# Kernel optimization log

Measured on AMD Instinct MI355X. Metric: run time of the kernel, lower is better.

The kernel has to match this reference:

```python
import jax, jax.numpy as jnp
import numpy as np

D_MODEL = 256
KSIZE = 16
EPS = 1e-5


def conv1d(x, w, b):
    # x: [B, C, N], w: [O, C, K], SAME padding over node axis
    y = jax.lax.conv_general_dilated(x, w, window_strides=(1,), padding='SAME',
                                     dimension_numbers=('NCH', 'OIH', 'NCH'))
    return y + b[None, :, None]


def layernorm(x, g, b):
    mu = jnp.mean(x, axis=-1, keepdims=True)
    var = jnp.mean(jnp.square(x - mu), axis=-1, keepdims=True)
    return (x - mu) * jax.lax.rsqrt(var + EPS) * g + b


def setup_inputs() -> dict:
    key = jax.random.key(0)
    ks = jax.random.split(key, 16)
    B, N, d, K = 4, 2048, D_MODEL, KSIZE
    conv_scale = 1.0 / np.sqrt(d * K)
    lin_scale = 1.0 / np.sqrt(d)
    return {
        'src': jax.random.normal(ks[0], (B, N, d), jnp.float32),
        'x_lst': jnp.zeros((B, N, N), jnp.float32),
        'adj': jax.random.randint(ks[1], (B, N, N), 0, 2, jnp.int32),
        'dis': jax.random.uniform(ks[2], (B, N, N), jnp.float32),
        'Wq': jax.random.normal(ks[3], (d, d, K), jnp.float32) * conv_scale,
        'bq': jnp.zeros((d,), jnp.float32),
        'Wk': jax.random.normal(ks[4], (d, d, K), jnp.float32) * conv_scale,
        'bk': jnp.zeros((d,), jnp.float32),
        'Wv': jax.random.normal(ks[5], (d, d, K), jnp.float32) * conv_scale,
        'bv': jnp.zeros((d,), jnp.float32),
        'W1': jax.random.normal(ks[6], (d, d), jnp.float32) * lin_scale,
        'b1': jnp.zeros((d,), jnp.float32),
        'W2': jax.random.normal(ks[7], (d, d), jnp.float32) * lin_scale,
        'b2': jnp.zeros((d,), jnp.float32),
        'W3': jax.random.normal(ks[8], (d, d), jnp.float32) * lin_scale,
        'b3': jnp.zeros((d,), jnp.float32),
        'g1': jnp.ones((d,), jnp.float32),
        'be1': jnp.zeros((d,), jnp.float32),
        'g2': jnp.ones((d,), jnp.float32),
        'be2': jnp.zeros((d,), jnp.float32),
    }


def reference(src, x_lst, adj, dis, Wq, bq, Wk, bk, Wv, bv,
              W1, b1, W2, b2, W3, b3, g1, be1, g2, be2):
    # ---- _ga_block: transpose to channel-major, graph attention ----
    x = jnp.swapaxes(src, -2, -1)                      # [B, d, N]
    q = conv1d(x, Wq, bq)                              # [B, d, N]
    k = conv1d(x, Wk, bk)
    v = conv1d(x, Wv, bv)
    scale = 1.0 / jnp.sqrt(jnp.asarray(D_MODEL, src.dtype))
    scores = jnp.einsum('bdn,bdm->bnm', q, k) * scale  # [B, N, N]
    scores = scores - dis                              # distance bias
    scores = jnp.where(adj > 0, scores, jnp.asarray(-1e9, scores.dtype))
    attn = jax.nn.softmax(scores, axis=-1)             # [B, N, N]
    x_lst_new = x_lst + attn                           # accumulated attention state
    out = jnp.einsum('bnm,bdm->bdn', attn, v)          # [B, d, N]
    x1 = jnp.swapaxes(out, -2, -1)                     # [B, N, d] (dropout = identity in eval)
    # ---- residual + norm1 ----
    h = layernorm(src + x1, g1, be1)
    # ---- 3-layer LeakyReLU MLP + residual + norm2 ----
    m = jax.nn.leaky_relu(h @ W1.T + b1)
    m = jax.nn.leaky_relu(m @ W2.T + b2)
    m = m @ W3.T + b3
    h = layernorm(h + m, g2, be2)
    return h, x_lst_new
```

## Files before the change

kernel.cpp:

```cpp
#include <hip/hip_runtime.h>
#include <stdint.h>

typedef _Float16 h16;
typedef _Float16 h8v __attribute__((ext_vector_type(8)));
typedef float    f4v __attribute__((ext_vector_type(4)));
typedef int      i4v __attribute__((ext_vector_type(4)));

#define NBATCH 4
#define NNODE  2048
#define DM     256
#define NPAD   2063
#define PARTN  (8192 * 256)

__device__ __forceinline__ void async16(const void* g, void* l) {
#if __has_builtin(__builtin_amdgcn_global_load_lds)
  __builtin_amdgcn_global_load_lds((__attribute__((address_space(1))) void*)g,
                                   (__attribute__((address_space(3))) void*)l, 16, 0, 0);
#else
  *(f4v*)l = *(const f4v*)g;
#endif
}

__device__ __forceinline__ void gemm_tile(
    const h16* Abase, int astride,
    const h16* Bbase, int bstride,
    h16* As, h16* Bs, f4v acc[4][4], int kiters)
{
  const int tid  = threadIdx.x;
  const int lane = tid & 63;
  const int wv   = tid >> 6;
  const int srow = tid >> 2;
  const int sch  = ((tid & 3) ^ ((tid >> 3) & 3)) * 8;
  const h16* gA0 = Abase + (long)srow * astride + sch;
  const h16* gA1 = Abase + (long)(srow + 64) * astride + sch;
  const h16* gB0 = Bbase + (long)srow * bstride + sch;
  const h16* gB1 = Bbase + (long)(srow + 64) * bstride + sch;
  h16* lA0 = As + tid * 8;
  h16* lA1 = As + 2048 + tid * 8;
  h16* lB0 = Bs + tid * 8;
  h16* lB1 = Bs + 2048 + tid * 8;
  const int swz = ((lane & 15) >> 1) & 3;
  const int qq  = ((lane >> 4) ^ swz) * 8;
  const int amr = ((wv & 1) * 64 + (lane & 15)) * 32 + qq;
  const int bnr = ((wv >> 1) * 64 + (lane & 15)) * 32 + qq;

  async16(gA0, lA0); async16(gA1, lA1);
  async16(gB0, lB0); async16(gB1, lB1);

  for (int kt = 0; kt < kiters; ++kt) {
    asm volatile("s_waitcnt vmcnt(0)" ::: "memory");
    __syncthreads();
    const int cur = (kt & 1) << 12;
    if (kt + 1 < kiters) {
      const int nxt = (~kt & 1) << 12;
      const int k0 = (kt + 1) * 32;
      async16(gA0 + k0, lA0 + nxt); async16(gA1 + k0, lA1 + nxt);
      async16(gB0 + k0, lB0 + nxt); async16(gB1 + k0, lB1 + nxt);
    }
    h8v af[4], bf[4];
#pragma unroll
    for (int i = 0; i < 4; ++i) af[i] = *(const h8v*)(As + cur + amr + i * 512);
#pragma unroll
    for (int j = 0; j < 4; ++j) bf[j] = *(const h8v*)(Bs + cur + bnr + j * 512);
#pragma unroll
    for (int i = 0; i < 4; ++i)
#pragma unroll
      for (int j = 0; j < 4; ++j)
        acc[i][j] = __builtin_amdgcn_mfma_f32_16x16x32_f16(af[i], bf[j], acc[i][j], 0, 0, 0);
  }
}

__device__ __forceinline__ void zero_acc(f4v acc[4][4]) {
#pragma unroll
  for (int i = 0; i < 4; ++i)
#pragma unroll
    for (int j = 0; j < 4; ++j) {
      f4v z = {0.f, 0.f, 0.f, 0.f};
      acc[i][j] = z;
    }
}

__global__ void prep_src_kernel(const float* __restrict__ src, h16* __restrict__ Xpad) {
  int idx = blockIdx.x * 256 + threadIdx.x;
  int c = idx & 255;
  int row = idx >> 8;
  int b = row / NPAD;
  int n = row - b * NPAD;
  float v = 0.f;
  int ns = n - 7;
  if (ns >= 0 && ns < NNODE) v = src[((long)b * NNODE + ns) * DM + c];
  Xpad[idx] = (h16)v;
}

__global__ void prep_wconv_kernel(const float* __restrict__ Wq, const float* __restrict__ Wk,
                                  const float* __restrict__ Wv, h16* __restrict__ Wt) {
  int idx = blockIdx.x * 256 + threadIdx.x;
  int w = idx >> 20;
  int rem = idx & 1048575;
  int o = rem >> 12;
  int tc = rem & 4095;
  int t = tc >> 8;
  int c = tc & 255;
  const float* W = (w == 0) ? Wq : (w == 1) ? Wk : Wv;
  Wt[idx] = (h16)W[(o * 256 + c) * 16 + t];
}

__global__ void prep_wlin_kernel(const float* __restrict__ W1, const float* __restrict__ W2,
                                 const float* __restrict__ W3, h16* __restrict__ Wl) {
  int idx = blockIdx.x * 256 + threadIdx.x;
  int w = idx >> 16;
  int rem = idx & 65535;
  const float* W = (w == 0) ? W1 : (w == 1) ? W2 : W3;
  Wl[idx] = (h16)W[rem];
}

__global__ __launch_bounds__(256) void conv_gemm_kernel(
    const h16* __restrict__ Xpad, const h16* __restrict__ Wt,
    const float* __restrict__ bq, const float* __restrict__ bk, const float* __restrict__ bv,
    h16* __restrict__ Q, h16* __restrict__ Ko, h16* __restrict__ Vt)
{
  __shared__ __align__(16) h16 As[8192];
  __shared__ __align__(16) h16 Bs[8192];
  const int mt = blockIdx.x, ct = blockIdx.y, w = blockIdx.z;
  const int m0 = mt * 128;
  const int b = m0 >> 11, n0 = m0 & 2047;
  const h16* Abase = Xpad + ((long)(b * NPAD + n0)) * DM;
  const h16* Bbase = Wt + (long)w * (256 * 4096) + (long)ct * 128 * 4096;
  f4v acc[4][4];
  zero_acc(acc);
  gemm_tile(Abase, DM, Bbase, 4096, As, Bs, acc, 128);

  const float* bias = (w == 0) ? bq : (w == 1) ? bk : bv;
  const int lane = threadIdx.x & 63, wv = threadIdx.x >> 6;
  const int rbase = (wv & 1) * 64 + (lane >> 4) * 4;
  const int cbase = (wv >> 1) * 64 + (lane & 15);
#pragma unroll
  for (int j = 0; j < 4; ++j) {
    const int gc = ct * 128 + cbase + j * 16;
    const float bias_v = bias[gc];
#pragma unroll
    for (int i = 0; i < 4; ++i) {
#pragma unroll
      for (int e = 0; e < 4; ++e) {
        const int gr = m0 + rbase + i * 16 + e;
        const float v = acc[i][j][e] + bias_v;
        if (w == 2) {
          const int bb = gr >> 11, n = gr & 2047;
          Vt[((long)(bb * 256 + gc)) * 2048 + n] = (h16)v;
        } else {
          h16* dst = (w == 0) ? Q : Ko;
          dst[(long)gr * 256 + gc] = (h16)v;
        }
      }
    }
  }
}

__global__ __launch_bounds__(256) void scores_gemm_kernel(
    const h16* __restrict__ Q, const h16* __restrict__ Km, h16* __restrict__ Sh)
{
  __shared__ __align__(16) h16 As[8192];
  __shared__ __align__(16) h16 Bs[8192];
  const int nt = blockIdx.x, mt = blockIdx.y, b = blockIdx.z;
  const h16* Abase = Q + ((long)b * NNODE + nt * 128) * 256;
  const h16* Bbase = Km + ((long)b * NNODE + mt * 128) * 256;
  f4v acc[4][4];
  zero_acc(acc);
  gemm_tile(Abase, 256, Bbase, 256, As, Bs, acc, 8);

  const int lane = threadIdx.x & 63, wv = threadIdx.x >> 6;
  const int rbase = (wv & 1) * 64 + (lane >> 4) * 4;
  const int cbase = (wv >> 1) * 64 + (lane & 15);
  h16* Srow = Sh + (long)b * NNODE * NNODE;
#pragma unroll
  for (int i = 0; i < 4; ++i) {
#pragma unroll
    for (int e = 0; e < 4; ++e) {
      const long row = nt * 128 + rbase + i * 16 + e;
#pragma unroll
      for (int j = 0; j < 4; ++j) {
        const int col = mt * 128 + cbase + j * 16;
        Srow[row * 2048 + col] = (h16)(acc[i][j][e] * 0.0625f);
      }
    }
  }
}

__device__ __forceinline__ float wred_max(float v) {
#pragma unroll
  for (int off = 32; off > 0; off >>= 1) v = fmaxf(v, __shfl_xor(v, off, 64));
  return v;
}
__device__ __forceinline__ float wred_sum(float v) {
#pragma unroll
  for (int off = 32; off > 0; off >>= 1) v += __shfl_xor(v, off, 64);
  return v;
}

__global__ __launch_bounds__(256) void softmax_kernel(
    h16* __restrict__ Sh, const float* __restrict__ dis, const int* __restrict__ adj,
    const float* __restrict__ x_lst, float* __restrict__ out_x)
{
  const int r = blockIdx.x;
  const long ro = (long)r * 2048;
  const int tid = threadIdx.x, lane = tid & 63, wv = tid >> 6;
  const int j0 = tid * 8;
  __shared__ float wmax[4], wsum[4];

  h8v sv = *(const h8v*)(Sh + ro + j0);
  f4v d0 = *(const f4v*)(dis + ro + j0);
  f4v d1 = *(const f4v*)(dis + ro + j0 + 4);
  i4v a0 = *(const i4v*)(adj + ro + j0);
  i4v a1 = *(const i4v*)(adj + ro + j0 + 4);

  float s[8];
#pragma unroll
  for (int k = 0; k < 4; ++k) s[k]     = (a0[k] > 0) ? ((float)sv[k]     - d0[k]) : -1e9f;
#pragma unroll
  for (int k = 0; k < 4; ++k) s[k + 4] = (a1[k] > 0) ? ((float)sv[k + 4] - d1[k]) : -1e9f;

  float m = s[0];
#pragma unroll
  for (int k = 1; k < 8; ++k) m = fmaxf(m, s[k]);
  m = wred_max(m);
  if (lane == 0) wmax[wv] = m;
  __syncthreads();
  m = fmaxf(fmaxf(wmax[0], wmax[1]), fmaxf(wmax[2], wmax[3]));

  float p[8], ls = 0.f;
#pragma unroll
  for (int k = 0; k < 8; ++k) { p[k] = __expf(s[k] - m); ls += p[k]; }
  ls = wred_sum(ls);
  if (lane == 0) wsum[wv] = ls;
  __syncthreads();
  const float inv = 1.0f / (wsum[0] + wsum[1] + wsum[2] + wsum[3]);

  f4v x0 = *(const f4v*)(x_lst + ro + j0);
  f4v x1 = *(const f4v*)(x_lst + ro + j0 + 4);
  f4v o0, o1;
  h8v pv;
#pragma unroll
  for (int k = 0; k < 4; ++k) {
    const float a = p[k] * inv, bq = p[k + 4] * inv;
    o0[k] = x0[k] + a; o1[k] = x1[k] + bq;
    pv[k] = (h16)a; pv[k + 4] = (h16)bq;
  }
  *(f4v*)(out_x + ro + j0) = o0;
  *(f4v*)(out_x + ro + j0 + 4) = o1;
  *(h8v*)(Sh + ro + j0) = pv;
}

__global__ __launch_bounds__(256) void av_gemm_kernel(
    const h16* __restrict__ Attn, const h16* __restrict__ Vt, float* __restrict__ X1p)
{
  __shared__ __align__(16) h16 As[8192];
  __shared__ __align__(16) h16 Bs[8192];
  const int nt = blockIdx.x, b = blockIdx.z;
  const int ct = blockIdx.y & 1, ks = blockIdx.y >> 1;
  const h16* Abase = Attn + ((long)b * NNODE + nt * 128) * 2048 + ks * 1024;
  const h16* Bbase = Vt + ((long)b * 256 + ct * 128) * 2048 + ks * 1024;
  f4v acc[4][4];
  zero_acc(acc);
  gemm_tile(Abase, 2048, Bbase, 2048, As, Bs, acc, 32);

  const int lane = threadIdx.x & 63, wv = threadIdx.x >> 6;
  const int rbase = (wv & 1) * 64 + (lane >> 4) * 4;
  const int cbase = (wv >> 1) * 64 + (lane & 15);
  float* dst = X1p + (long)ks * PARTN;
#pragma unroll
  for (int i = 0; i < 4; ++i) {
#pragma unroll
    for (int e = 0; e < 4; ++e) {
      const long row = (long)b * NNODE + nt * 128 + rbase + i * 16 + e;
#pragma unroll
      for (int j = 0; j < 4; ++j) {
        const int col = ct * 128 + cbase + j * 16;
        dst[row * 256 + col] = acc[i][j][e];
      }
    }
  }
}

__global__ __launch_bounds__(256) void mlp_gemm_kernel(
    const h16* __restrict__ A, const h16* __restrict__ W, const float* __restrict__ bias,
    h16* __restrict__ outH, float* __restrict__ outF)
{
  __shared__ __align__(16) h16 As[8192];
  __shared__ __align__(16) h16 Bs[8192];
  const int mt = blockIdx.x, ct = blockIdx.y;
  const h16* Abase = A + (long)mt * 128 * 256;
  const h16* Bbase = W + (long)ct * 128 * 256;
  f4v acc[4][4];
  zero_acc(acc);
  gemm_tile(Abase, 256, Bbase, 256, As, Bs, acc, 8);

  const int lane = threadIdx.x & 63, wv = threadIdx.x >> 6;
  const int rbase = (wv & 1) * 64 + (lane >> 4) * 4;
  const int cbase = (wv >> 1) * 64 + (lane & 15);
#pragma unroll
  for (int j = 0; j < 4; ++j) {
    const int gc = ct * 128 + cbase + j * 16;
    const float bias_v = bias[gc];
#pragma unroll
    for (int i = 0; i < 4; ++i) {
#pragma unroll
      for (int e = 0; e < 4; ++e) {
        const long gr = (long)mt * 128 + rbase + i * 16 + e;
        float v = acc[i][j][e] + bias_v;
        if (outH) {
          v = (v >= 0.f) ? v : 0.01f * v;
          outH[gr * 256 + gc] = (h16)v;
        } else {
          outF[gr * 256 + gc] = v;
        }
      }
    }
  }
}

__global__ __launch_bounds__(256) void ln_kernel(
    const float* __restrict__ X, const float* __restrict__ Y, const float* __restrict__ Y2,
    const float* __restrict__ g, const float* __restrict__ bb,
    float* __restrict__ outF, h16* __restrict__ outH)
{
  const int wv = threadIdx.x >> 6, lane = threadIdx.x & 63;
  const long r = (long)blockIdx.x * 4 + wv;
  const long off = r * 256 + lane * 4;
  f4v x = *(const f4v*)(X + off);
  f4v y = *(const f4v*)(Y + off);
  if (Y2) {
    f4v y2 = *(const f4v*)(Y2 + off);
#pragma unroll
    for (int k = 0; k < 4; ++k) y[k] += y2[k];
  }
  float v[4];
  float sum = 0.f, sq = 0.f;
#pragma unroll
  for (int k = 0; k < 4; ++k) { v[k] = x[k] + y[k]; sum += v[k]; sq += v[k] * v[k]; }
  sum = wred_sum(sum);
  sq  = wred_sum(sq);
  const float mu = sum * (1.0f / 256.0f);
  const float var = sq * (1.0f / 256.0f) - mu * mu;
  const float rs = rsqrtf(var + 1e-5f);
  f4v gg = *(const f4v*)(g + lane * 4);
  f4v be = *(const f4v*)(bb + lane * 4);
  f4v o;
#pragma unroll
  for (int k = 0; k < 4; ++k) o[k] = (v[k] - mu) * rs * gg[k] + be[k];
  if (outF) *(f4v*)(outF + off) = o;
  if (outH) {
    _Float16 hv[4];
#pragma unroll
    for (int k = 0; k < 4; ++k) hv[k] = (h16)o[k];
    *(ulong1*)(outH + off) = *(ulong1*)hv;
  }
}

extern "C" void kernel_launch(void* const* d_in, const int* in_sizes, int n_in,
                              void* d_out, int out_size, void* d_ws, size_t ws_size,
                              hipStream_t stream)
{
  const float* src  = (const float*)d_in[0];
  const float* xlst = (const float*)d_in[1];
  const int*   adj  = (const int*)d_in[2];
  const float* dis  = (const float*)d_in[3];
  const float* Wq   = (const float*)d_in[4];
  const float* bq   = (const float*)d_in[5];
  const float* Wk   = (const float*)d_in[6];
  const float* bk   = (const float*)d_in[7];
  const float* Wv   = (const float*)d_in[8];
  const float* bvp  = (const float*)d_in[9];
  const float* W1   = (const float*)d_in[10];
  const float* b1   = (const float*)d_in[11];
  const float* W2   = (const float*)d_in[12];
  const float* b2   = (const float*)d_in[13];
  const float* W3   = (const float*)d_in[14];
  const float* b3   = (const float*)d_in[15];
  const float* g1   = (const float*)d_in[16];
  const float* be1  = (const float*)d_in[17];
  const float* g2   = (const float*)d_in[18];
  const float* be2  = (const float*)d_in[19];
  (void)in_sizes; (void)n_in; (void)out_size; (void)ws_size;

  char* ws = (char*)d_ws;
  size_t off = 0;
  auto alloc = [&](size_t bytes) -> void* {
    void* p = ws + off;
    off += (bytes + 1023) & ~(size_t)1023;
    return p;
  };
  h16*   Xpad = (h16*)  alloc((size_t)NBATCH * NPAD * DM * 2);
  h16*   Wt   = (h16*)  alloc((size_t)3 * 256 * 4096 * 2);
  h16*   Wl   = (h16*)  alloc((size_t)3 * 256 * 256 * 2);
  h16*   Qb   = (h16*)  alloc((size_t)NBATCH * NNODE * DM * 2);
  h16*   Kb   = (h16*)  alloc((size_t)NBATCH * NNODE * DM * 2);
  h16*   Vt   = (h16*)  alloc((size_t)NBATCH * DM * NNODE * 2);
  h16*   Sh   = (h16*)  alloc((size_t)NBATCH * NNODE * NNODE * 2);
  float* X1p  = (float*)alloc((size_t)2 * PARTN * 4);
  float* H    = (float*)alloc((size_t)NBATCH * NNODE * DM * 4);
  h16*   H16  = (h16*)  alloc((size_t)NBATCH * NNODE * DM * 2);
  h16*   M1   = (h16*)  alloc((size_t)NBATCH * NNODE * DM * 2);
  h16*   M2   = (h16*)  alloc((size_t)NBATCH * NNODE * DM * 2);
  float* M3   = X1p;

  float* out_h = (float*)d_out;
  float* out_x = out_h + (size_t)NBATCH * NNODE * DM;

  prep_src_kernel<<<(NBATCH * NPAD * DM) / 256, 256, 0, stream>>>(src, Xpad);
  prep_wconv_kernel<<<(3 * 256 * 4096) / 256, 256, 0, stream>>>(Wq, Wk, Wv, Wt);
  prep_wlin_kernel<<<(3 * 256 * 256) / 256, 256, 0, stream>>>(W1, W2, W3, Wl);

  conv_gemm_kernel<<<dim3(64, 2, 3), 256, 0, stream>>>(Xpad, Wt, bq, bk, bvp, Qb, Kb, Vt);
  scores_gemm_kernel<<<dim3(16, 16, 4), 256, 0, stream>>>(Qb, Kb, Sh);
  softmax_kernel<<<NBATCH * NNODE, 256, 0, stream>>>(Sh, dis, adj, xlst, out_x);
  av_gemm_kernel<<<dim3(16, 4, 4), 256, 0, stream>>>(Sh, Vt, X1p);
  ln_kernel<<<(NBATCH * NNODE) / 4, 256, 0, stream>>>(src, X1p, X1p + PARTN, g1, be1, H, H16);
  mlp_gemm_kernel<<<dim3(64, 2), 256, 0, stream>>>(H16, Wl, b1, M1, nullptr);
  mlp_gemm_kernel<<<dim3(64, 2), 256, 0, stream>>>(M1, Wl + 65536, b2, M2, nullptr);
  mlp_gemm_kernel<<<dim3(64, 2), 256, 0, stream>>>(M2, Wl + 2 * 65536, b3, nullptr, M3);
  ln_kernel<<<(NBATCH * NNODE) / 4, 256, 0, stream>>>(H, M3, nullptr, g2, be2, out_h, nullptr);
}
```

Baseline: 482.1 us.

## Split-K the conv GEMM, single-buffer GEMM tiles, and coalesce weight transpose

The conv GEMM is split four ways along K, giving 1536 blocks instead of 384. It writes fp16 partials, and a new reduce kernel sums them and adds the biases. The shared GEMM tile loop drops LDS double-buffering in favour of a synchronous load-wait-compute loop, which halves shared memory per block and may raise occupancy but gives up load/compute overlap in every GEMM. The conv weight transpose now goes through LDS so reads and writes are coalesced, and the workspace is aliased so the partial buffers share memory with the scores buffer. Keeping the partials in fp16 adds rounding error, and the extra reduce pass adds memory traffic.

```diff
diff --git a/kernel.cpp b/kernel.cpp
--- a/kernel.cpp
+++ b/kernel.cpp
@@ -10,6 +10,7 @@
 #define NNODE  2048
 #define DM     256
 #define NPAD   2063
+#define QKELEM 2097152
 #define PARTN  (8192 * 256)
 
 __device__ __forceinline__ void async16(const void* g, void* l) {
@@ -44,24 +45,20 @@
   const int amr = ((wv & 1) * 64 + (lane & 15)) * 32 + qq;
   const int bnr = ((wv >> 1) * 64 + (lane & 15)) * 32 + qq;
 
-  async16(gA0, lA0); async16(gA1, lA1);
-  async16(gB0, lB0); async16(gB1, lB1);
-
   for (int kt = 0; kt < kiters; ++kt) {
+    const int k0 = kt * 32;
+    __syncthreads();
+    async16(gA0 + k0, lA0);
+    async16(gA1 + k0, lA1);
+    async16(gB0 + k0, lB0);
+    async16(gB1 + k0, lB1);
     asm volatile("s_waitcnt vmcnt(0)" ::: "memory");
     __syncthreads();
-    const int cur = (kt & 1) << 12;
-    if (kt + 1 < kiters) {
-      const int nxt = (~kt & 1) << 12;
-      const int k0 = (kt + 1) * 32;
-      async16(gA0 + k0, lA0 + nxt); async16(gA1 + k0, lA1 + nxt);
-      async16(gB0 + k0, lB0 + nxt); async16(gB1 + k0, lB1 + nxt);
-    }
     h8v af[4], bf[4];
 #pragma unroll
-    for (int i = 0; i < 4; ++i) af[i] = *(const h8v*)(As + cur + amr + i * 512);
-#pragma unroll
-    for (int j = 0; j < 4; ++j) bf[j] = *(const h8v*)(Bs + cur + bnr + j * 512);
+    for (int i = 0; i < 4; ++i) af[i] = *(const h8v*)(As + amr + i * 512);
+#pragma unroll
+    for (int j = 0; j < 4; ++j) bf[j] = *(const h8v*)(Bs + bnr + j * 512);
 #pragma unroll
     for (int i = 0; i < 4; ++i)
 #pragma unroll
@@ -92,17 +89,31 @@
   Xpad[idx] = (h16)v;
 }
 
-__global__ void prep_wconv_kernel(const float* __restrict__ Wq, const float* __restrict__ Wk,
-                                  const float* __restrict__ Wv, h16* __restrict__ Wt) {
-  int idx = blockIdx.x * 256 + threadIdx.x;
-  int w = idx >> 20;
-  int rem = idx & 1048575;
-  int o = rem >> 12;
-  int tc = rem & 4095;
-  int t = tc >> 8;
-  int c = tc & 255;
+__global__ __launch_bounds__(256) void prep_wconv_kernel(
+    const float* __restrict__ Wq, const float* __restrict__ Wk,
+    const float* __restrict__ Wv, h16* __restrict__ Wt)
+{
+  __shared__ float lds[16][257];
+  const int w = blockIdx.x >> 8, o = blockIdx.x & 255, tid = threadIdx.x;
   const float* W = (w == 0) ? Wq : (w == 1) ? Wk : Wv;
-  Wt[idx] = (h16)W[(o * 256 + c) * 16 + t];
+  const float* base = W + (long)o * 4096;
+  f4v r0 = *(const f4v*)(base + tid * 16);
+  f4v r1 = *(const f4v*)(base + tid * 16 + 4);
+  f4v r2 = *(const f4v*)(base + tid * 16 + 8);
+  f4v r3 = *(const f4v*)(base + tid * 16 + 12);
+#pragma unroll
+  for (int k = 0; k < 4; ++k) {
+    lds[k][tid] = r0[k]; lds[4 + k][tid] = r1[k];
+    lds[8 + k][tid] = r2[k]; lds[12 + k][tid] = r3[k];
+  }
+  __syncthreads();
+  const int t = tid >> 4, c0 = (tid & 15) * 16;
+  h16* out = Wt + ((long)(w * 256 + o)) * 4096 + t * 256 + c0;
+  h8v o0, o1;
+#pragma unroll
+  for (int k = 0; k < 8; ++k) { o0[k] = (h16)lds[t][c0 + k]; o1[k] = (h16)lds[t][c0 + 8 + k]; }
+  *(h8v*)out = o0;
+  *(h8v*)(out + 8) = o1;
 }
 
 __global__ void prep_wlin_kernel(const float* __restrict__ W1, const float* __restrict__ W2,
@@ -116,51 +127,89 @@
 
 __global__ __launch_bounds__(256) void conv_gemm_kernel(
     const h16* __restrict__ Xpad, const h16* __restrict__ Wt,
-    const float* __restrict__ bq, const float* __restrict__ bk, const float* __restrict__ bv,
-    h16* __restrict__ Q, h16* __restrict__ Ko, h16* __restrict__ Vt)
-{
-  __shared__ __align__(16) h16 As[8192];
-  __shared__ __align__(16) h16 Bs[8192];
-  const int mt = blockIdx.x, ct = blockIdx.y, w = blockIdx.z;
+    h16* __restrict__ Qp, h16* __restrict__ Kp, h16* __restrict__ Vp)
+{
+  __shared__ __align__(16) h16 As[4096];
+  __shared__ __align__(16) h16 Bs[4096];
+  const int mt = blockIdx.x, ct = blockIdx.y;
+  const int w = blockIdx.z >> 2, ks = blockIdx.z & 3;
   const int m0 = mt * 128;
   const int b = m0 >> 11, n0 = m0 & 2047;
-  const h16* Abase = Xpad + ((long)(b * NPAD + n0)) * DM;
-  const h16* Bbase = Wt + (long)w * (256 * 4096) + (long)ct * 128 * 4096;
+  const h16* Abase = Xpad + ((long)(b * NPAD + n0)) * DM + ks * 1024;
+  const h16* Bbase = Wt + (long)w * (256 * 4096) + (long)ct * 128 * 4096 + ks * 1024;
   f4v acc[4][4];
   zero_acc(acc);
-  gemm_tile(Abase, DM, Bbase, 4096, As, Bs, acc, 128);
-
-  const float* bias = (w == 0) ? bq : (w == 1) ? bk : bv;
+  gemm_tile(Abase, DM, Bbase, 4096, As, Bs, acc, 32);
+
+  h16* dst = ((w == 0) ? Qp : (w == 1) ? Kp : Vp) + (long)ks * QKELEM;
   const int lane = threadIdx.x & 63, wv = threadIdx.x >> 6;
   const int rbase = (wv & 1) * 64 + (lane >> 4) * 4;
   const int cbase = (wv >> 1) * 64 + (lane & 15);
 #pragma unroll
   for (int j = 0; j < 4; ++j) {
     const int gc = ct * 128 + cbase + j * 16;
-    const float bias_v = bias[gc];
 #pragma unroll
     for (int i = 0; i < 4; ++i) {
 #pragma unroll
       for (int e = 0; e < 4; ++e) {
         const int gr = m0 + rbase + i * 16 + e;
-        const float v = acc[i][j][e] + bias_v;
+        const h16 v = (h16)acc[i][j][e];
         if (w == 2) {
           const int bb = gr >> 11, n = gr & 2047;
-          Vt[((long)(bb * 256 + gc)) * 2048 + n] = (h16)v;
+          dst[((long)(bb * 256 + gc)) * 2048 + n] = v;
         } else {
-          h16* dst = (w == 0) ? Q : Ko;
-          dst[(long)gr * 256 + gc] = (h16)v;
+          dst[(long)gr * 256 + gc] = v;
         }
       }
     }
   }
 }
 
+__global__ __launch_bounds__(256) void conv_reduce_kernel(
+    const h16* __restrict__ Qp, const h16* __restrict__ Kp, const h16* __restrict__ Vp,
+    const float* __restrict__ bq, const float* __restrict__ bk, const float* __restrict__ bv,
+    h16* __restrict__ Qb, h16* __restrict__ Kb, h16* __restrict__ Vt)
+{
+  const long gid = (long)blockIdx.x * 256 + threadIdx.x;
+  if (gid < 2 * (QKELEM / 8)) {
+    const int which = gid >= (QKELEM / 8);
+    const long e = (gid - (long)which * (QKELEM / 8)) * 8;
+    const h16* P = which ? Kp : Qp;
+    const float* bias = which ? bk : bq;
+    float s[8] = {0.f, 0.f, 0.f, 0.f, 0.f, 0.f, 0.f, 0.f};
+#pragma unroll
+    for (int ks = 0; ks < 4; ++ks) {
+      h8v p = *(const h8v*)(P + (long)ks * QKELEM + e);
+#pragma unroll
+      for (int k = 0; k < 8; ++k) s[k] += (float)p[k];
+    }
+    const int c0 = (int)(e & 255);
+    h8v o;
+#pragma unroll
+    for (int k = 0; k < 8; ++k) o[k] = (h16)(s[k] + bias[c0 + k]);
+    *(h8v*)((which ? Kb : Qb) + e) = o;
+  } else {
+    const long e = (gid - 2 * (QKELEM / 8)) * 8;
+    float s[8] = {0.f, 0.f, 0.f, 0.f, 0.f, 0.f, 0.f, 0.f};
+#pragma unroll
+    for (int ks = 0; ks < 4; ++ks) {
+      h8v p = *(const h8v*)(Vp + (long)ks * QKELEM + e);
+#pragma unroll
+      for (int k = 0; k < 8; ++k) s[k] += (float)p[k];
+    }
+    const float bias_v = bv[(int)((e >> 11) & 255)];
+    h8v o;
+#pragma unroll
+    for (int k = 0; k < 8; ++k) o[k] = (h16)(s[k] + bias_v);
+    *(h8v*)(Vt + e) = o;
+  }
+}
+
 __global__ __launch_bounds__(256) void scores_gemm_kernel(
     const h16* __restrict__ Q, const h16* __restrict__ Km, h16* __restrict__ Sh)
 {
-  __shared__ __align__(16) h16 As[8192];
-  __shared__ __align__(16) h16 Bs[8192];
+  __shared__ __align__(16) h16 As[4096];
+  __shared__ __align__(16) h16 Bs[4096];
   const int nt = blockIdx.x, mt = blockIdx.y, b = blockIdx.z;
   const h16* Abase = Q + ((long)b * NNODE + nt * 128) * 256;
   const h16* Bbase = Km + ((long)b * NNODE + mt * 128) * 256;
@@ -253,8 +302,8 @@
 __global__ __launch_bounds__(256) void av_gemm_kernel(
     const h16* __restrict__ Attn, const h16* __restrict__ Vt, float* __restrict__ X1p)
 {
-  __shared__ __align__(16) h16 As[8192];
-  __shared__ __align__(16) h16 Bs[8192];
+  __shared__ __align__(16) h16 As[4096];
+  __shared__ __align__(16) h16 Bs[4096];
   const int nt = blockIdx.x, b = blockIdx.z;
   const int ct = blockIdx.y & 1, ks = blockIdx.y >> 1;
   const h16* Abase = Attn + ((long)b * NNODE + nt * 128) * 2048 + ks * 1024;
@@ -285,8 +334,8 @@
     const h16* __restrict__ A, const h16* __restrict__ W, const float* __restrict__ bias,
     h16* __restrict__ outH, float* __restrict__ outF)
 {
-  __shared__ __align__(16) h16 As[8192];
-  __shared__ __align__(16) h16 Bs[8192];
+  __shared__ __align__(16) h16 As[4096];
+  __shared__ __align__(16) h16 Bs[4096];
   const int mt = blockIdx.x, ct = blockIdx.y;
   const h16* Abase = A + (long)mt * 128 * 256;
   const h16* Bbase = W + (long)ct * 128 * 256;
@@ -392,25 +441,31 @@
   h16*   Xpad = (h16*)  alloc((size_t)NBATCH * NPAD * DM * 2);
   h16*   Wt   = (h16*)  alloc((size_t)3 * 256 * 4096 * 2);
   h16*   Wl   = (h16*)  alloc((size_t)3 * 256 * 256 * 2);
-  h16*   Qb   = (h16*)  alloc((size_t)NBATCH * NNODE * DM * 2);
-  h16*   Kb   = (h16*)  alloc((size_t)NBATCH * NNODE * DM * 2);
-  h16*   Vt   = (h16*)  alloc((size_t)NBATCH * DM * NNODE * 2);
-  h16*   Sh   = (h16*)  alloc((size_t)NBATCH * NNODE * NNODE * 2);
-  float* X1p  = (float*)alloc((size_t)2 * PARTN * 4);
-  float* H    = (float*)alloc((size_t)NBATCH * NNODE * DM * 4);
-  h16*   H16  = (h16*)  alloc((size_t)NBATCH * NNODE * DM * 2);
-  h16*   M1   = (h16*)  alloc((size_t)NBATCH * NNODE * DM * 2);
-  h16*   M2   = (h16*)  alloc((size_t)NBATCH * NNODE * DM * 2);
+  h16*   Qb   = (h16*)  alloc((size_t)QKELEM * 2);
+  h16*   Kb   = (h16*)  alloc((size_t)QKELEM * 2);
+  h16*   Vt   = (h16*)  alloc((size_t)QKELEM * 2);
+  char*  R    = (char*) alloc((size_t)71400 * 1024);
+  h16*   Qp   = (h16*)R;
+  h16*   Kp   = (h16*)(R + (size_t)4 * QKELEM * 2);
+  h16*   Vp   = (h16*)(R + (size_t)8 * QKELEM * 2);
+  h16*   Sh   = (h16*)R;
+  float* X1p  = (float*)(R + (size_t)16 * QKELEM);
+  float* H    = (float*)(R + (size_t)16 * QKELEM + (size_t)2 * PARTN * 4);
+  h16*   H16  = (h16*)((char*)H + (size_t)PARTN * 4);
+  h16*   M1   = (h16*)((char*)H16 + (size_t)PARTN * 2);
+  h16*   M2   = (h16*)((char*)M1 + (size_t)PARTN * 2);
   float* M3   = X1p;
 
   float* out_h = (float*)d_out;
   float* out_x = out_h + (size_t)NBATCH * NNODE * DM;
 
   prep_src_kernel<<<(NBATCH * NPAD * DM) / 256, 256, 0, stream>>>(src, Xpad);
-  prep_wconv_kernel<<<(3 * 256 * 4096) / 256, 256, 0, stream>>>(Wq, Wk, Wv, Wt);
+  prep_wconv_kernel<<<3 * 256, 256, 0, stream>>>(Wq, Wk, Wv, Wt);
   prep_wlin_kernel<<<(3 * 256 * 256) / 256, 256, 0, stream>>>(W1, W2, W3, Wl);
 
-  conv_gemm_kernel<<<dim3(64, 2, 3), 256, 0, stream>>>(Xpad, Wt, bq, bk, bvp, Qb, Kb, Vt);
+  conv_gemm_kernel<<<dim3(64, 2, 12), 256, 0, stream>>>(Xpad, Wt, Qp, Kp, Vp);
+  conv_reduce_kernel<<<3 * (QKELEM / 8) / 256, 256, 0, stream>>>(
+      Qp, Kp, Vp, bq, bk, bvp, Qb, Kb, Vt);
   scores_gemm_kernel<<<dim3(16, 16, 4), 256, 0, stream>>>(Qb, Kb, Sh);
   softmax_kernel<<<NBATCH * NNODE, 256, 0, stream>>>(Sh, dis, adj, xlst, out_x);
   av_gemm_kernel<<<dim3(16, 4, 4), 256, 0, stream>>>(Sh, Vt, X1p);
```

New measurement: 462.8 us. -4.0%, faster.
